# Optimization experiments

Hardware: AMD Instinct MI355X
Metric: run time of the kernel (lower is better)

## Reference

```python
import jax, jax.numpy as jnp
import numpy as np

T = 2048      # num_tokens == max_seq_len
D = 4096      # d_in
H = 32        # num_heads
G = 8         # num_kv_groups
HD = 128      # head_dim
GS = H // G   # group_size = 4
EPS = 1e-6


def _make_rope(t, hd):
    inv_freq = 1.0 / (10000.0 ** (np.arange(0, hd, 2, dtype=np.float64) / hd))
    freqs = np.outer(np.arange(t, dtype=np.float64), inv_freq)      # [T, HD/2]
    emb = np.concatenate([freqs, freqs], axis=-1)                   # [T, HD]
    return (jnp.asarray(np.cos(emb), jnp.float32),
            jnp.asarray(np.sin(emb), jnp.float32))


def setup_inputs() -> dict:
    key = jax.random.key(0)
    ks = jax.random.split(key, 6)
    x = jax.random.normal(ks[0], (T, D), jnp.float32)
    # causal mask: True = masked (upper triangle above diagonal)
    mask = jnp.triu(jnp.ones((T, T), jnp.bool_), k=1)
    cos, sin = _make_rope(T, HD)
    s = 0.02
    Wq = jax.random.normal(ks[1], (D, H * HD), jnp.float32) * s
    Wk = jax.random.normal(ks[2], (D, G * HD), jnp.float32) * s
    Wv = jax.random.normal(ks[3], (D, G * HD), jnp.float32) * s
    Wo = jax.random.normal(ks[4], (H * HD, D), jnp.float32) * s
    qn_w = jnp.ones((HD,), jnp.float32)
    kn_w = jnp.ones((HD,), jnp.float32)
    return {"x": x, "mask": mask, "cos": cos, "sin": sin,
            "Wq": Wq, "Wk": Wk, "Wv": Wv, "Wo": Wo,
            "qn_w": qn_w, "kn_w": kn_w}


def _rmsnorm(u, w):
    # normalize over head_dim (last axis), eps inside sqrt
    var = jnp.mean(jnp.square(u), axis=-1, keepdims=True)
    return u * jax.lax.rsqrt(var + EPS) * w


def _rope(u, cos, sin):
    # rotate-half RoPE; u: [heads, T, HD], cos/sin: [T, HD]
    hd = u.shape[-1]
    u1, u2 = u[..., : hd // 2], u[..., hd // 2:]
    rot = jnp.concatenate([-u2, u1], axis=-1)
    return u * cos[None] + rot * sin[None]


def reference(x, mask, cos, sin, Wq, Wk, Wv, Wo, qn_w, kn_w):
    t = x.shape[0]
    q = (x @ Wq).reshape(t, H, HD).transpose(1, 0, 2)   # [H, T, HD]
    k = (x @ Wk).reshape(t, G, HD).transpose(1, 0, 2)   # [G, T, HD]
    v = (x @ Wv).reshape(t, G, HD).transpose(1, 0, 2)   # [G, T, HD]
    q = _rmsnorm(q, qn_w)
    k = _rmsnorm(k, kn_w)
    q = _rope(q, cos, sin)
    k = _rope(k, cos, sin)
    # GQA expansion: repeat_interleave along head axis
    k = jnp.repeat(k, GS, axis=0)                       # [H, T, HD]
    v = jnp.repeat(v, GS, axis=0)                       # [H, T, HD]
    scores = jnp.einsum('hqd,hkd->hqk', q, k) / (HD ** 0.5)
    scores = jnp.where(mask[None], -jnp.inf, scores)
    w = jax.nn.softmax(scores, axis=-1)
    attn = jnp.einsum('hqk,hkd->hqd', w, v)             # [H, T, HD]
    attn = attn.transpose(1, 0, 2).reshape(t, H * HD)
    return attn @ Wo
```

## Files before the change

### kernel.cpp

```cpp
#include <hip/hip_runtime.h>

#define T_ 2048
#define D_ 4096
#define H_ 32
#define G_ 8
#define HD_ 128

typedef float f32x4 __attribute__((ext_vector_type(4)));
typedef __bf16 bf16x8 __attribute__((ext_vector_type(8)));
typedef unsigned short u16x8 __attribute__((ext_vector_type(8)));
typedef unsigned short u16x4 __attribute__((ext_vector_type(4)));

__device__ __forceinline__ unsigned short f2bf(float f) {
  unsigned u = __builtin_bit_cast(unsigned, f);
  u += 0x7FFFu + ((u >> 16) & 1u);
  return (unsigned short)(u >> 16);
}
__device__ __forceinline__ float bf2f(unsigned short h) {
  return __builtin_bit_cast(float, (unsigned)h << 16);
}

__device__ __forceinline__ void gload_lds16(const unsigned short* g, unsigned short* l) {
  __builtin_amdgcn_global_load_lds((const __attribute__((address_space(1))) void*)g,
                                   (__attribute__((address_space(3))) void*)l, 16, 0, 0);
}

__global__ __launch_bounds__(256) void convert_bf16(const float* __restrict__ in,
                                                    unsigned short* __restrict__ out) {
  const size_t i = ((size_t)blockIdx.x * 256 + threadIdx.x) * 8;
  float4 a = *(const float4*)(in + i);
  float4 b = *(const float4*)(in + i + 4);
  u16x8 o;
  o[0] = f2bf(a.x); o[1] = f2bf(a.y); o[2] = f2bf(a.z); o[3] = f2bf(a.w);
  o[4] = f2bf(b.x); o[5] = f2bf(b.y); o[6] = f2bf(b.z); o[7] = f2bf(b.w);
  *(u16x8*)(out + i) = o;
}

__global__ __launch_bounds__(256) void transpose_convert(const float* __restrict__ Wm,
                                                         unsigned short* __restrict__ Wt,
                                                         int R, int C) {
  __shared__ float tile[64][65];
  const int r0 = blockIdx.x * 64, c0 = blockIdx.y * 64;
  const int lr4 = threadIdx.x >> 6, lc = threadIdx.x & 63;
#pragma unroll
  for (int i = 0; i < 16; ++i) {
    int r = i * 4 + lr4;
    tile[r][lc] = Wm[(size_t)(r0 + r) * C + c0 + lc];
  }
  __syncthreads();
#pragma unroll
  for (int i = 0; i < 16; ++i) {
    int r = i * 4 + lr4;
    Wt[(size_t)(c0 + r) * R + r0 + lc] = f2bf(tile[lc][r]);
  }
}

__global__ __launch_bounds__(256) void transpose_convert_qkv(const float* __restrict__ Wq,
                                                             const float* __restrict__ Wk,
                                                             const float* __restrict__ Wv,
                                                             unsigned short* __restrict__ Wt) {
  __shared__ float tile[64][65];
  const int r0 = blockIdx.x * 64;
  const int cg = blockIdx.y * 64;
  const float* Wm;
  int C, c0;
  if (cg < 4096)      { Wm = Wq; C = 4096; c0 = cg; }
  else if (cg < 5120) { Wm = Wk; C = 1024; c0 = cg - 4096; }
  else                { Wm = Wv; C = 1024; c0 = cg - 5120; }
  const int lr4 = threadIdx.x >> 6, lc = threadIdx.x & 63;
#pragma unroll
  for (int i = 0; i < 16; ++i) {
    int r = i * 4 + lr4;
    tile[r][lc] = Wm[(size_t)(r0 + r) * C + c0 + lc];
  }
  __syncthreads();
#pragma unroll
  for (int i = 0; i < 16; ++i) {
    int r = i * 4 + lr4;
    Wt[(size_t)(cg + r) * 4096 + r0 + lc] = f2bf(tile[lc][r]);
  }
}

__global__ __launch_bounds__(256) void transpose_v(const unsigned short* __restrict__ v,
                                                   unsigned short* __restrict__ vt, int stride) {
  __shared__ unsigned short tile[64][65];
  const int t0 = blockIdx.x * 64, d0 = blockIdx.y * 64, g = blockIdx.z;
  const int lr4 = threadIdx.x >> 6, lc = threadIdx.x & 63;
#pragma unroll
  for (int i = 0; i < 16; ++i) {
    int r = i * 4 + lr4;
    tile[r][lc] = v[(size_t)(t0 + r) * stride + g * HD_ + d0 + lc];
  }
  __syncthreads();
#pragma unroll
  for (int i = 0; i < 16; ++i) {
    int r = i * 4 + lr4;
    vt[((size_t)g * HD_ + d0 + r) * T_ + t0 + lc] = tile[lc][r];
  }
}

__global__ __launch_bounds__(256) void norm_rope2(const unsigned short* __restrict__ qkv,
                                                  unsigned short* __restrict__ qout,
                                                  unsigned short* __restrict__ kout,
                                                  const float* __restrict__ qw,
                                                  const float* __restrict__ kw,
                                                  const float* __restrict__ cs,
                                                  const float* __restrict__ sn) {
  int bid = blockIdx.x;
  const unsigned short* raw;
  unsigned short* outp;
  const float* w;
  int NH;
  if (bid < 16384) { raw = qkv;        outp = qout; w = qw; NH = 32; }
  else             { raw = qkv + 4096; outp = kout; w = kw; NH = 8; bid -= 16384; }
  const int row = bid * 4 + (threadIdx.x >> 6);
  const int lane = threadIdx.x & 63;
  const int t = row / NH, h = row - t * NH;
  const unsigned short* src = raw + (size_t)t * 6144 + h * HD_;
  float u1 = bf2f(src[lane]);
  float u2 = bf2f(src[lane + 64]);
  float ss = u1 * u1 + u2 * u2;
#pragma unroll
  for (int m = 1; m < 64; m <<= 1) ss += __shfl_xor(ss, m);
  float rr = rsqrtf(ss * (1.f / 128.f) + 1e-6f);
  float c = cs[(size_t)t * HD_ + lane];
  float s = sn[(size_t)t * HD_ + lane];
  float a = u1 * rr * w[lane];
  float b = u2 * rr * w[lane + 64];
  unsigned short* dst = outp + ((size_t)h * T_ + t) * HD_;
  dst[lane]      = f2bf(a * c - b * s);
  dst[lane + 64] = f2bf(b * c + a * s);
}

template <int NFW, int HALF>
__device__ __forceinline__ void mfma_h(f32x4 (&acc)[4][NFW], bf16x8 (&af)[4][2],
                                       bf16x8 (&bf)[NFW / 2][2]) {
  __builtin_amdgcn_s_setprio(1);
#pragma unroll
  for (int fm = 0; fm < 4; ++fm)
#pragma unroll
    for (int j = 0; j < NFW / 2; ++j) {
      constexpr int base = HALF * (NFW / 2);
      f32x4 a = acc[fm][base + j];
      a = __builtin_amdgcn_mfma_f32_16x16x32_bf16(af[fm][0], bf[j][0], a, 0, 0, 0);
      a = __builtin_amdgcn_mfma_f32_16x16x32_bf16(af[fm][1], bf[j][1], a, 0, 0, 0);
      acc[fm][base + j] = a;
    }
  __builtin_amdgcn_s_setprio(0);
}

template <int NFW, int OUTF32>
__global__ __launch_bounds__(256, 2) void gemm4(const unsigned short* __restrict__ A,
                                                const unsigned short* __restrict__ Bt,
                                                void* __restrict__ Cv, int M, int N,
                                                int K, int LDA) {
  constexpr int BN = 32 * NFW;
  constexpr int ABUF = 8192;
  constexpr int BBUF = BN * 64;
  __shared__ __align__(16) unsigned short lds[2 * ABUF + 2 * BBUF];
  const int tid = threadIdx.x;
  const int wid = tid >> 6, lane = tid & 63;
  const int lr = lane & 15, lhi = lane >> 4;
  const int wr = wid >> 1, wcn = wid & 1;

  int flat = blockIdx.y * gridDim.x + blockIdx.x;
  int nwg = gridDim.x * gridDim.y;
  int swz = (flat & 7) * (nwg >> 3) + (flat >> 3);
  const int brow = (swz & 15) * 128;
  const int bcol = (swz >> 4) * BN;

  const int nt = K >> 6;

  f32x4 acc[4][NFW];
#pragma unroll
  for (int b = 0; b < 4; ++b)
#pragma unroll
    for (int c = 0; c < NFW; ++c) acc[b][c] = (f32x4){0.f, 0.f, 0.f, 0.f};

  const int t8 = tid >> 3;
  const int srcCol = ((tid & 7) ^ (t8 & 7)) * 8;
  auto stageA = [&](int d, int u, int ktp) {
#pragma unroll
    for (int l = 0; l < 2; ++l)
      gload_lds16(A + (size_t)(brow + u * 64 + l * 32 + t8) * LDA + ktp * 64 + srcCol,
                  &lds[d * ABUF + u * 4096 + l * 2048 + tid * 8]);
  };
  auto stageB = [&](int d, int v, int ktp) {
#pragma unroll
    for (int l = 0; l < 2; ++l)
      gload_lds16(Bt + (size_t)(bcol + v * 64 + l * 32 + t8) * LDA + ktp * 64 + srcCol,
                  &lds[2 * ABUF + d * BBUF + v * 4096 + l * 2048 + tid * 8]);
  };

  bf16x8 af[4][2], bf[NFW / 2][2];
  auto readA = [&](int d) {
#pragma unroll
    for (int fm = 0; fm < 4; ++fm) {
      int row = wr * 64 + fm * 16 + lr;
      int base = d * ABUF + row * 64;
      int sw = (row & 7) << 3;
      af[fm][0] = *(const bf16x8*)&lds[base + ((lhi * 8) ^ sw)];
      af[fm][1] = *(const bf16x8*)&lds[base + ((32 + lhi * 8) ^ sw)];
    }
  };
  auto readBf = [&](int d, int fn, bf16x8 (&slot)[2]) {
    int row = wcn * (16 * NFW) + fn * 16 + lr;
    int base = 2 * ABUF + d * BBUF + row * 64;
    int sw = (row & 7) << 3;
    slot[0] = *(const bf16x8*)&lds[base + ((lhi * 8) ^ sw)];
    slot[1] = *(const bf16x8*)&lds[base + ((32 + lhi * 8) ^ sw)];
  };

  stageA(0, 0, 0); stageA(0, 1, 0);
#pragma unroll
  for (int v = 0; v < NFW / 2; ++v) stageB(0, v, 0);
  stageA(1, 0, 1); stageA(1, 1, 1);
  asm volatile("s_waitcnt vmcnt(4)" ::: "memory");
  __builtin_amdgcn_s_barrier();

  for (int t = 0; t < nt; ++t) {
    const int d = t & 1, dn = d ^ 1;
    readA(d);
#pragma unroll
    for (int j = 0; j < NFW / 2; ++j) readBf(d, j, bf[j]);
    if (t + 1 < nt) {
#pragma unroll
      for (int v = 0; v < NFW / 2; ++v) stageB(dn, v, t + 1);
    }
    __builtin_amdgcn_s_barrier();
    mfma_h<NFW, 0>(acc, af, bf);
    __builtin_amdgcn_s_barrier();
#pragma unroll
    for (int j = 0; j < NFW / 2; ++j) readBf(d, NFW / 2 + j, bf[j]);
    if (t + 2 < nt) { stageA(d, 0, t + 2); stageA(d, 1, t + 2); }
    __builtin_amdgcn_s_barrier();
    mfma_h<NFW, 1>(acc, af, bf);
    if (t < nt - 2) asm volatile("s_waitcnt vmcnt(4)" ::: "memory");
    else if (t == nt - 2) asm volatile("s_waitcnt vmcnt(0)" ::: "memory");
    __builtin_amdgcn_s_barrier();
  }

#pragma unroll
  for (int fm = 0; fm < 4; ++fm)
#pragma unroll
    for (int fn = 0; fn < NFW; ++fn) {
      int col = bcol + wcn * (16 * NFW) + fn * 16 + lr;
#pragma unroll
      for (int r = 0; r < 4; ++r) {
        int row = brow + wr * 64 + fm * 16 + lhi * 4 + r;
        if (OUTF32)
          ((float*)Cv)[(size_t)row * N + col] = acc[fm][fn][r];
        else
          ((unsigned short*)Cv)[(size_t)row * N + col] = f2bf(acc[fm][fn][r]);
      }
    }
}

__global__ __launch_bounds__(512) void flash_attn(const unsigned short* __restrict__ q,
                                                  const unsigned short* __restrict__ k,
                                                  const unsigned short* __restrict__ vt,
                                                  unsigned short* __restrict__ attnb) {
  const int pairIdx = blockIdx.y;
  const int g = pairIdx >> 1;
  const int qcp = blockIdx.x;
  const int tid = threadIdx.x;
  const int wid = tid >> 6;
  const int lane = tid & 63;
  const int lr = lane & 15, lhi = lane >> 4;
  const int h = pairIdx * 2 + (wid >> 2);

  __shared__ __align__(16) unsigned short Ks[2][64 * HD_];
  __shared__ __align__(16) unsigned short Vs[2][HD_ * 64];
  __shared__ __align__(16) unsigned short p_lds_all[8][16 * 64];
  unsigned short* p_lds = p_lds_all[wid];

  const unsigned short* kg = k + (size_t)g * T_ * HD_;
  const unsigned short* vg = vt + (size_t)g * HD_ * T_;

  int ko[2], vo[2];
#pragma unroll
  for (int p = 0; p < 2; ++p) {
    int ob = (p * 512 + tid) * 16;
    int krow = ob >> 8, kb = ob & 255;
    ko[p] = krow * HD_ + ((kb ^ ((krow & 7) << 4)) >> 1);
    int vrow = ob >> 7, vb2 = ob & 127;
    vo[p] = vrow * T_ + ((vb2 ^ ((vrow & 7) << 4)) >> 1);
  }
  const int lbase = wid * 512;

  const int sx = (lr & 7) << 4;
  const float scale2 = 0.08838834764831845f * 1.4426950408889634f;

  for (int pass = 0; pass < 2; ++pass) {
    const int qc = pass ? (31 - qcp) : qcp;
    const int q0 = qc * 64 + (wid & 3) * 16;

    bf16x8 qf[4];
    {
      const unsigned short* qrow = q + ((size_t)h * T_ + q0 + lr) * HD_ + lhi * 8;
#pragma unroll
      for (int c = 0; c < 4; ++c) qf[c] = *(const bf16x8*)(qrow + c * 32);
    }
    f32x4 accO[8];
#pragma unroll
    for (int i = 0; i < 8; ++i) accO[i] = (f32x4){0.f, 0.f, 0.f, 0.f};
    float mrow = -3e38f;
    float lrow = 0.f;

    const int ntile = qc + 1;

#pragma unroll
    for (int p = 0; p < 2; ++p) {
      gload_lds16(kg + ko[p], &Ks[0][p * 4096 + lbase]);
      gload_lds16(vg + vo[p], &Vs[0][p * 4096 + lbase]);
    }
    __syncthreads();

    for (int kt = 0; kt < ntile; ++kt) {
      const int b = kt & 1;
      const int kv0 = kt << 6;
      if (kt + 1 < ntile) {
        const size_t kofs = (size_t)(kv0 + 64) * HD_;
#pragma unroll
        for (int p = 0; p < 2; ++p) {
          gload_lds16(kg + kofs + ko[p], &Ks[b ^ 1][p * 4096 + lbase]);
          gload_lds16(vg + (kv0 + 64) + vo[p], &Vs[b ^ 1][p * 4096 + lbase]);
        }
      }
      f32x4 st[4];
      __builtin_amdgcn_s_setprio(1);
#pragma unroll
      for (int j = 0; j < 4; ++j) {
        st[j] = (f32x4){0.f, 0.f, 0.f, 0.f};
        const int krow = j * 16 + lr;
#pragma unroll
        for (int c = 0; c < 4; ++c) {
          bf16x8 kf = *(const bf16x8*)&Ks[b][krow * HD_ + (((c * 64 + lhi * 16) ^ sx) >> 1)];
          st[j] = __builtin_amdgcn_mfma_f32_16x16x32_bf16(kf, qf[c], st[j], 0, 0, 0);
        }
      }
      __builtin_amdgcn_s_setprio(0);
      if (kt == ntile - 1) {
#pragma unroll
        for (int j = 0; j < 4; ++j)
#pragma unroll
          for (int r = 0; r < 4; ++r)
            st[j][r] = (kv0 + j * 16 + lhi * 4 + r <= q0 + lr) ? st[j][r] * scale2 : -3e38f;
      } else {
#pragma unroll
        for (int j = 0; j < 4; ++j)
#pragma unroll
          for (int r = 0; r < 4; ++r) st[j][r] *= scale2;
      }
      float pm = st[0][0];
#pragma unroll
      for (int j = 0; j < 4; ++j)
#pragma unroll
        for (int r = 0; r < 4; ++r) pm = fmaxf(pm, st[j][r]);
      pm = fmaxf(pm, __shfl_xor(pm, 16));
      pm = fmaxf(pm, __shfl_xor(pm, 32));
      if (!__all(pm - mrow <= 8.f)) {
        float mnew = fmaxf(mrow, pm);
        float al = __builtin_amdgcn_exp2f(mrow - mnew);
        mrow = mnew;
        lrow *= al;
        float a0 = __shfl(al, lhi * 4 + 0);
        float a1 = __shfl(al, lhi * 4 + 1);
        float a2 = __shfl(al, lhi * 4 + 2);
        float a3 = __shfl(al, lhi * 4 + 3);
#pragma unroll
        for (int dt = 0; dt < 8; ++dt) {
          accO[dt][0] *= a0; accO[dt][1] *= a1; accO[dt][2] *= a2; accO[dt][3] *= a3;
        }
      }
      float ps = 0.f;
#pragma unroll
      for (int j = 0; j < 4; ++j)
#pragma unroll
        for (int r = 0; r < 4; ++r) {
          float e = __builtin_amdgcn_exp2f(st[j][r] - mrow);
          st[j][r] = e;
          ps += e;
        }
      ps += __shfl_xor(ps, 16);
      ps += __shfl_xor(ps, 32);
      lrow += ps;
#pragma unroll
      for (int j = 0; j < 4; ++j) {
        u16x4 pw;
        pw[0] = f2bf(st[j][0]); pw[1] = f2bf(st[j][1]);
        pw[2] = f2bf(st[j][2]); pw[3] = f2bf(st[j][3]);
        *(u16x4*)&p_lds[lr * 64 + (((j * 32 + lhi * 8) ^ sx) >> 1)] = pw;
      }
      bf16x8 pa0 = *(const bf16x8*)&p_lds[lr * 64 + (((lhi * 16) ^ sx) >> 1)];
      bf16x8 pa1 = *(const bf16x8*)&p_lds[lr * 64 + (((64 + lhi * 16) ^ sx) >> 1)];
      __builtin_amdgcn_s_setprio(1);
#pragma unroll
      for (int dt = 0; dt < 8; ++dt) {
        const int vrow = dt * 16 + lr;
        bf16x8 vf0 = *(const bf16x8*)&Vs[b][vrow * 64 + (((lhi * 16) ^ sx) >> 1)];
        bf16x8 vf1 = *(const bf16x8*)&Vs[b][vrow * 64 + (((64 + lhi * 16) ^ sx) >> 1)];
        accO[dt] = __builtin_amdgcn_mfma_f32_16x16x32_bf16(pa0, vf0, accO[dt], 0, 0, 0);
        accO[dt] = __builtin_amdgcn_mfma_f32_16x16x32_bf16(pa1, vf1, accO[dt], 0, 0, 0);
      }
      __builtin_amdgcn_s_setprio(0);
      __syncthreads();
    }
    float rinv = 1.f / lrow;
    float i0 = __shfl(rinv, lhi * 4 + 0);
    float i1 = __shfl(rinv, lhi * 4 + 1);
    float i2 = __shfl(rinv, lhi * 4 + 2);
    float i3 = __shfl(rinv, lhi * 4 + 3);
    float iv[4] = {i0, i1, i2, i3};
#pragma unroll
    for (int r = 0; r < 4; ++r) {
      size_t rowoff = (size_t)(q0 + lhi * 4 + r) * (H_ * HD_) + h * HD_;
#pragma unroll
      for (int dt = 0; dt < 8; ++dt) attnb[rowoff + dt * 16 + lr] = f2bf(accO[dt][r] * iv[r]);
    }
  }
}

extern "C" void kernel_launch(void* const* d_in, const int* in_sizes, int n_in,
                              void* d_out, int out_size, void* d_ws, size_t ws_size,
                              hipStream_t stream) {
  const float* x = (const float*)d_in[0];
  const float* cosT = (const float*)d_in[2];
  const float* sinT = (const float*)d_in[3];
  const float* Wq = (const float*)d_in[4];
  const float* Wk = (const float*)d_in[5];
  const float* Wv = (const float*)d_in[6];
  const float* Wo = (const float*)d_in[7];
  const float* qn = (const float*)d_in[8];
  const float* kn = (const float*)d_in[9];

  unsigned char* w = (unsigned char*)d_ws;
  unsigned short* xb     = (unsigned short*)(w);
  unsigned short* WqkvT  = (unsigned short*)(w + 16777216);
  unsigned short* qkvraw = (unsigned short*)(w + 67108864);
  unsigned short* qbuf   = (unsigned short*)(w + 92274688);
  unsigned short* kbuf   = (unsigned short*)(w + 109051904);
  unsigned short* vtb    = (unsigned short*)(w + 113246208);
  unsigned short* WoT    = WqkvT;
  unsigned short* attnb  = xb;

  convert_bf16<<<dim3(4096), dim3(256), 0, stream>>>(x, xb);
  transpose_convert_qkv<<<dim3(64, 96), dim3(256), 0, stream>>>(Wq, Wk, Wv, WqkvT);

  gemm4<6, 0><<<dim3(16, 32), dim3(256), 0, stream>>>(xb, WqkvT, (void*)qkvraw, 2048, 6144, 4096, 4096);

  norm_rope2<<<dim3(20480), dim3(256), 0, stream>>>(qkvraw, qbuf, kbuf, qn, kn, cosT, sinT);
  transpose_v<<<dim3(32, 2, 8), dim3(256), 0, stream>>>(qkvraw + 5120, vtb, 6144);
  transpose_convert<<<dim3(64, 64), dim3(256), 0, stream>>>(Wo, WoT, 4096, 4096);

  flash_attn<<<dim3(16, 16), dim3(512), 0, stream>>>(qbuf, kbuf, vtb, attnb);

  gemm4<4, 1><<<dim3(16, 32), dim3(256), 0, stream>>>(attnb, WoT, d_out, 2048, 4096, 4096, 4096);
}
```

Baseline: 319.7 us.

## Load all B fragments upfront and drop intermediate barriers in GEMM loop

Reads both halves of the B fragments from LDS before any MFMA work, instead of reloading the second half between two compute phases. This removes two workgroup barriers per k-iteration and the s_setprio priority hints, leaving one barrier before the A prefetch overwrites the current buffer. It aims to cut synchronisation stalls and let MFMA overlap more with LDS and global traffic, at the cost of more live registers for the extra B fragments.

```diff
diff --git a/kernel.cpp b/kernel.cpp
--- a/kernel.cpp
+++ b/kernel.cpp
@@ -132,23 +132,6 @@
   dst[lane + 64] = f2bf(b * c + a * s);
 }
 
-template <int NFW, int HALF>
-__device__ __forceinline__ void mfma_h(f32x4 (&acc)[4][NFW], bf16x8 (&af)[4][2],
-                                       bf16x8 (&bf)[NFW / 2][2]) {
-  __builtin_amdgcn_s_setprio(1);
-#pragma unroll
-  for (int fm = 0; fm < 4; ++fm)
-#pragma unroll
-    for (int j = 0; j < NFW / 2; ++j) {
-      constexpr int base = HALF * (NFW / 2);
-      f32x4 a = acc[fm][base + j];
-      a = __builtin_amdgcn_mfma_f32_16x16x32_bf16(af[fm][0], bf[j][0], a, 0, 0, 0);
-      a = __builtin_amdgcn_mfma_f32_16x16x32_bf16(af[fm][1], bf[j][1], a, 0, 0, 0);
-      acc[fm][base + j] = a;
-    }
-  __builtin_amdgcn_s_setprio(0);
-}
-
 template <int NFW, int OUTF32>
 __global__ __launch_bounds__(256, 2) void gemm4(const unsigned short* __restrict__ A,
                                                 const unsigned short* __restrict__ Bt,
@@ -157,6 +140,7 @@
   constexpr int BN = 32 * NFW;
   constexpr int ABUF = 8192;
   constexpr int BBUF = BN * 64;
+  constexpr int NH = NFW / 2;
   __shared__ __align__(16) unsigned short lds[2 * ABUF + 2 * BBUF];
   const int tid = threadIdx.x;
   const int wid = tid >> 6, lane = tid & 63;
@@ -192,7 +176,7 @@
                   &lds[2 * ABUF + d * BBUF + v * 4096 + l * 2048 + tid * 8]);
   };
 
-  bf16x8 af[4][2], bf[NFW / 2][2];
+  bf16x8 af[4][2], bfL[NH][2], bfU[NH][2];
   auto readA = [&](int d) {
 #pragma unroll
     for (int fm = 0; fm < 4; ++fm) {
@@ -213,7 +197,7 @@
 
   stageA(0, 0, 0); stageA(0, 1, 0);
 #pragma unroll
-  for (int v = 0; v < NFW / 2; ++v) stageB(0, v, 0);
+  for (int v = 0; v < NH; ++v) stageB(0, v, 0);
   stageA(1, 0, 1); stageA(1, 1, 1);
   asm volatile("s_waitcnt vmcnt(4)" ::: "memory");
   __builtin_amdgcn_s_barrier();
@@ -222,19 +206,33 @@
     const int d = t & 1, dn = d ^ 1;
     readA(d);
 #pragma unroll
-    for (int j = 0; j < NFW / 2; ++j) readBf(d, j, bf[j]);
+    for (int j = 0; j < NH; ++j) readBf(d, j, bfL[j]);
+#pragma unroll
+    for (int j = 0; j < NH; ++j) readBf(d, NH + j, bfU[j]);
     if (t + 1 < nt) {
 #pragma unroll
-      for (int v = 0; v < NFW / 2; ++v) stageB(dn, v, t + 1);
-    }
+      for (int v = 0; v < NH; ++v) stageB(dn, v, t + 1);
+    }
+#pragma unroll
+    for (int fm = 0; fm < 4; ++fm)
+#pragma unroll
+      for (int j = 0; j < NH; ++j) {
+        f32x4 a = acc[fm][j];
+        a = __builtin_amdgcn_mfma_f32_16x16x32_bf16(af[fm][0], bfL[j][0], a, 0, 0, 0);
+        a = __builtin_amdgcn_mfma_f32_16x16x32_bf16(af[fm][1], bfL[j][1], a, 0, 0, 0);
+        acc[fm][j] = a;
+      }
     __builtin_amdgcn_s_barrier();
-    mfma_h<NFW, 0>(acc, af, bf);
-    __builtin_amdgcn_s_barrier();
-#pragma unroll
-    for (int j = 0; j < NFW / 2; ++j) readBf(d, NFW / 2 + j, bf[j]);
     if (t + 2 < nt) { stageA(d, 0, t + 2); stageA(d, 1, t + 2); }
-    __builtin_amdgcn_s_barrier();
-    mfma_h<NFW, 1>(acc, af, bf);
+#pragma unroll
+    for (int fm = 0; fm < 4; ++fm)
+#pragma unroll
+      for (int j = 0; j < NH; ++j) {
+        f32x4 a = acc[fm][NH + j];
+        a = __builtin_amdgcn_mfma_f32_16x16x32_bf16(af[fm][0], bfU[j][0], a, 0, 0, 0);
+        a = __builtin_amdgcn_mfma_f32_16x16x32_bf16(af[fm][1], bfU[j][1], a, 0, 0, 0);
+        acc[fm][NH + j] = a;
+      }
     if (t < nt - 2) asm volatile("s_waitcnt vmcnt(4)" ::: "memory");
     else if (t == nt - 2) asm volatile("s_waitcnt vmcnt(0)" ::: "memory");
     __builtin_amdgcn_s_barrier();
```

Result: no change. 317.5 us, median of 2 (-0.7%).
